# Performance work log

Hardware: AMD Instinct MI355X
Metric: run time of the kernel (lower is better)

## Reference

```python
import jax, jax.numpy as jnp
import numpy as np

C, H, W = 16, 512, 512
HID = 128
N_STEPS = 8


def setup_inputs() -> dict:
    key = jax.random.key(0)
    k1, k2, k3 = jax.random.split(key, 3)
    state = jax.random.normal(k1, (C, H, W), dtype=jnp.float32)
    # MLP params: 5*C = 80 gathered features -> HID -> C delta channels
    W1 = jax.random.normal(k2, (5 * C, HID), dtype=jnp.float32) * (1.0 / np.sqrt(5 * C))
    b1 = jnp.zeros((HID,), dtype=jnp.float32)
    W2 = jax.random.normal(k3, (HID, C), dtype=jnp.float32) * (1.0 / np.sqrt(HID))
    b2 = jnp.zeros((C,), dtype=jnp.float32)
    return {"state": state, "W1": W1, "b1": b1, "W2": W2, "b2": b2, "n_steps": N_STEPS}


def _neighbor_idx(n):
    i = jnp.arange(n)
    minus = jnp.maximum(i - 1, 0)          # clamp at low edge (cy==0 -> 0)
    plus = jnp.where(i == n - 1, 0, i + 1)  # WRAP to 0 at high edge (original quirk)
    return minus, plus


def reference(state, W1, b1, W2, b2, n_steps):
    c, h, w = state.shape
    up, down = _neighbor_idx(h)
    left, right = _neighbor_idx(w)

    def step(s, _):
        # von-Neumann gather: (5C, H, W), feature order [center, up, down, left, right]
        feats = jnp.concatenate(
            [s, s[:, up, :], s[:, down, :], s[:, :, left], s[:, :, right]], axis=0)
        x = feats.reshape(5 * c, h * w).T        # (HW, 5C)
        hdn = jax.nn.relu(x @ W1 + b1)           # (HW, HID)
        delta = (hdn @ W2 + b2).T.reshape(c, h, w)
        s_new = s + delta
        s_new = s_new.at[0].set(s[0])            # channel 0 snapshot restore
        return s_new, None

    out, _ = jax.lax.scan(step, state, None, length=n_steps)
    return out
```

## Files before the change

### kernel.cpp

```cpp
#include <hip/hip_runtime.h>
#include <hip/hip_bf16.h>

#define HH 512
#define WW 512
#define CC 16
#define HIDN 128
#define HWSZ (HH*WW)

typedef __attribute__((ext_vector_type(8))) short short8;
typedef __attribute__((ext_vector_type(4))) short short4v;
typedef __attribute__((ext_vector_type(4))) float float4v;

__device__ __forceinline__ short to_bf16(float f){
    __hip_bfloat16 h = __float2bfloat16(f);
    return __builtin_bit_cast(short, h);
}

__global__ void __launch_bounds__(256) prep_kernel(
    const float* __restrict__ W1, const float* __restrict__ W2,
    short* __restrict__ w1t, short* __restrict__ w2t)
{
    int t = blockIdx.x * blockDim.x + threadIdx.x;
    int stride = gridDim.x * blockDim.x;
    for (int idx = t; idx < HIDN*96; idx += stride){
        int n = idx / 96;
        int k = idx - n*96;
        float v = (k < 80) ? W1[k*HIDN + n] : 0.0f;
        w1t[idx] = to_bf16(v);
    }
    for (int idx = t; idx < CC*HIDN; idx += stride){
        int n = idx >> 7;
        int k = idx & 127;
        w2t[idx] = to_bf16(W2[k*CC + n]);
    }
}

#define RSTRIDE 24
#define RROW    (68*RSTRIDE)

__global__ void __launch_bounds__(256, 5) step_kernel(
    const float* __restrict__ src, float* __restrict__ dst,
    const short* __restrict__ w1t, const short* __restrict__ w2t,
    const float* __restrict__ b1, const float* __restrict__ b2)
{
    __shared__ __align__(16) short rows_u[3*RROW];
    __shared__ __align__(16) short hdn[64][136];

    const int t    = threadIdx.x;
    const int w    = t >> 6;
    const int lane = t & 63;
    const int ln15 = lane & 15;
    const int g4   = lane >> 4;

    const int bx = blockIdx.x;
    const int y  = bx >> 3;
    const int xs = (bx & 7) << 6;

    const int yu = (y == 0)      ? 0 : (y - 1);
    const int yd = (y == HH - 1) ? 0 : (y + 1);

    if (t < 192){
        const int r  = t >> 6;
        const int l  = t & 63;
        const int q  = l & 15;
        const int cq = l >> 4;
        const int rowg = (r == 0) ? y : ((r == 1) ? yu : yd);
        const float* base = src + (size_t)rowg * WW + xs + (q << 2);
        float4v f[4];
        #pragma unroll
        for (int i = 0; i < 4; ++i)
            f[i] = *(const float4v*)(base + (size_t)((cq << 2) + i) * HWSZ);
        #pragma unroll
        for (int j = 0; j < 4; ++j){
            short4v v;
            v[0] = to_bf16(f[0][j]); v[1] = to_bf16(f[1][j]);
            v[2] = to_bf16(f[2][j]); v[3] = to_bf16(f[3][j]);
            *(short4v*)&rows_u[r*RROW + ((q << 2) + 1 + j)*RSTRIDE + (cq << 2)] = v;
        }
    } else if (t < 224){
        const int c    = (t - 192) & 15;
        const int side = (t - 192) >> 4;
        const int gx   = (side == 0) ? ((xs == 0) ? 0 : xs - 1)
                                     : ((xs + 64 == WW) ? 0 : xs + 64);
        rows_u[(side * 65)*RSTRIDE + c] =
            to_bf16(src[(size_t)c*HWSZ + (size_t)y*WW + gx]);
    }

    int offB[3];
    #pragma unroll
    for (int kk = 0; kk < 3; ++kk){
        const int g  = (kk < 2) ? ((kk << 2) + g4) : (8 + (g4 & 1));
        const int n  = g >> 1;
        const int cb = (g & 1) << 3;
        const int r  = (n == 1) ? 1 : ((n == 2) ? 2 : 0);
        const int dx = (n == 3) ? -1 : ((n == 4) ? 1 : 0);
        offB[kk] = r*RROW + (ln15 + 1 + dx)*RSTRIDE + cb;
    }

    __syncthreads();

    float4v acc[2][4];
    #pragma unroll
    for (int mt = 0; mt < 2; ++mt)
        #pragma unroll
        for (int nt = 0; nt < 4; ++nt)
            acc[mt][nt] = (float4v){0.f, 0.f, 0.f, 0.f};

    #pragma unroll
    for (int kk = 0; kk < 3; ++kk){
        short8 bfragF[4];
        #pragma unroll
        for (int nt = 0; nt < 4; ++nt)
            bfragF[nt] = *(const short8*)(&rows_u[offB[kk] + nt * (16 * RSTRIDE)]);
        #pragma unroll
        for (int mt = 0; mt < 2; ++mt){
            const int hrow = (((w << 1) + mt) << 4) + ln15;
            short8 afragW = *(const short8*)(w1t + hrow * 96 + (kk << 5) + (g4 << 3));
            #pragma unroll
            for (int nt = 0; nt < 4; ++nt)
                acc[mt][nt] = __builtin_amdgcn_mfma_f32_16x16x32_bf16(
                    afragW, bfragF[nt], acc[mt][nt], 0, 0, 0);
        }
    }

    #pragma unroll
    for (int mt = 0; mt < 2; ++mt){
        const int hbase = (((w << 1) + mt) << 4) + (g4 << 2);
        const float4v bb = *(const float4v*)(b1 + hbase);
        #pragma unroll
        for (int nt = 0; nt < 4; ++nt){
            short4v s;
            #pragma unroll
            for (int r = 0; r < 4; ++r){
                float v = acc[mt][nt][r] + bb[r];
                v = v > 0.f ? v : 0.f;
                s[r] = to_bf16(v);
            }
            *(short4v*)&hdn[(nt << 4) + ln15][hbase] = s;
        }
    }
    __syncthreads();

    const int pxb = (w << 4) + (g4 << 2);
    const size_t gofs = (size_t)ln15 * HWSZ + (size_t)y * WW + xs + pxb;
    const float4v sold = *(const float4v*)(src + gofs);
    const float bias2 = b2[ln15];

    float4v acc2 = (float4v){0.f, 0.f, 0.f, 0.f};
    #pragma unroll
    for (int kk = 0; kk < 4; ++kk){
        const int k0 = kk << 5;
        short8 a = *(const short8*)(&hdn[(w << 4) + ln15][k0 + (g4 << 3)]);
        short8 b = *(const short8*)(w2t + ln15 * HIDN + k0 + (g4 << 3));
        acc2 = __builtin_amdgcn_mfma_f32_16x16x32_bf16(a, b, acc2, 0, 0, 0);
    }

    float4v outv;
    #pragma unroll
    for (int r = 0; r < 4; ++r){
        const float v = sold[r] + acc2[r] + bias2;
        outv[r] = (ln15 == 0) ? sold[r] : v;
    }
    *(float4v*)(dst + gofs) = outv;
}

extern "C" void kernel_launch(void* const* d_in, const int* in_sizes, int n_in,
                              void* d_out, int out_size, void* d_ws, size_t ws_size,
                              hipStream_t stream)
{
    const float* state = (const float*)d_in[0];
    const float* W1    = (const float*)d_in[1];
    const float* b1    = (const float*)d_in[2];
    const float* W2    = (const float*)d_in[3];
    const float* b2    = (const float*)d_in[4];

    float* B1  = (float*)d_ws;
    short* w1t = (short*)((char*)d_ws + (size_t)HWSZ * CC * 4);
    short* w2t = w1t + HIDN * 96;
    float* out = (float*)d_out;

    prep_kernel<<<32, 256, 0, stream>>>(W1, W2, w1t, w2t);

    dim3 grid(HH * (WW / 64));
    step_kernel<<<grid, 256, 0, stream>>>(state, B1, w1t, w2t, b1, b2);
    step_kernel<<<grid, 256, 0, stream>>>(B1, out, w1t, w2t, b1, b2);
    step_kernel<<<grid, 256, 0, stream>>>(out, B1, w1t, w2t, b1, b2);
    step_kernel<<<grid, 256, 0, stream>>>(B1, out, w1t, w2t, b1, b2);
    step_kernel<<<grid, 256, 0, stream>>>(out, B1, w1t, w2t, b1, b2);
    step_kernel<<<grid, 256, 0, stream>>>(B1, out, w1t, w2t, b1, b2);
    step_kernel<<<grid, 256, 0, stream>>>(out, B1, w1t, w2t, b1, b2);
    step_kernel<<<grid, 256, 0, stream>>>(B1, out, w1t, w2t, b1, b2);
}
```

Measured before the change: 264.2 us.

## Give each wave all hidden units for its own pixels, dropping a barrier

The first MLP layer is re-partitioned. Before, each wave computed 32 hidden units for all 64 pixels of the block. Now each wave computes all 128 hidden units for its own 16 pixels, so the hidden tile it writes to LDS is read back only by the same wave and the second __syncthreads can go. The staged-row LDS layout is compacted so up and down rows need no halo padding, and the launch-bounds occupancy hint rises from 5 to 6 blocks. In exchange, each wave now loads 8 W1 fragments per k-step instead of 2, raising cache traffic for weights, and it relies on in-wave LDS ordering with no explicit barrier.

```diff
diff --git a/kernel.cpp b/kernel.cpp
--- a/kernel.cpp
+++ b/kernel.cpp
@@ -36,14 +36,17 @@
 }
 
 #define RSTRIDE 24
-#define RROW    (68*RSTRIDE)
+#define BASE_C  0
+#define BASE_U  (66*RSTRIDE)
+#define BASE_D  ((66+64)*RSTRIDE)
+#define RTOT    ((66+64+64)*RSTRIDE)
 
-__global__ void __launch_bounds__(256, 5) step_kernel(
+__global__ void __launch_bounds__(256, 6) step_kernel(
     const float* __restrict__ src, float* __restrict__ dst,
     const short* __restrict__ w1t, const short* __restrict__ w2t,
     const float* __restrict__ b1, const float* __restrict__ b2)
 {
-    __shared__ __align__(16) short rows_u[3*RROW];
+    __shared__ __align__(16) short rows_u[RTOT];
     __shared__ __align__(16) short hdn[64][136];
 
     const int t    = threadIdx.x;
@@ -65,6 +68,8 @@
         const int q  = l & 15;
         const int cq = l >> 4;
         const int rowg = (r == 0) ? y : ((r == 1) ? yu : yd);
+        const int pbase = (r == 0) ? BASE_C : ((r == 1) ? BASE_U : BASE_D);
+        const int xoff  = (r == 0) ? 1 : 0;
         const float* base = src + (size_t)rowg * WW + xs + (q << 2);
         float4v f[4];
         #pragma unroll
@@ -75,14 +80,14 @@
             short4v v;
             v[0] = to_bf16(f[0][j]); v[1] = to_bf16(f[1][j]);
             v[2] = to_bf16(f[2][j]); v[3] = to_bf16(f[3][j]);
-            *(short4v*)&rows_u[r*RROW + ((q << 2) + 1 + j)*RSTRIDE + (cq << 2)] = v;
+            *(short4v*)&rows_u[pbase + ((q << 2) + xoff + j)*RSTRIDE + (cq << 2)] = v;
         }
     } else if (t < 224){
         const int c    = (t - 192) & 15;
         const int side = (t - 192) >> 4;
         const int gx   = (side == 0) ? ((xs == 0) ? 0 : xs - 1)
                                      : ((xs + 64 == WW) ? 0 : xs + 64);
-        rows_u[(side * 65)*RSTRIDE + c] =
+        rows_u[BASE_C + (side * 65)*RSTRIDE + c] =
             to_bf16(src[(size_t)c*HWSZ + (size_t)y*WW + gx]);
     }
 
@@ -92,66 +97,60 @@
         const int g  = (kk < 2) ? ((kk << 2) + g4) : (8 + (g4 & 1));
         const int n  = g >> 1;
         const int cb = (g & 1) << 3;
-        const int r  = (n == 1) ? 1 : ((n == 2) ? 2 : 0);
-        const int dx = (n == 3) ? -1 : ((n == 4) ? 1 : 0);
-        offB[kk] = r*RROW + (ln15 + 1 + dx)*RSTRIDE + cb;
+        int o;
+        if (n == 1)      o = BASE_U + ln15*RSTRIDE;
+        else if (n == 2) o = BASE_D + ln15*RSTRIDE;
+        else {
+            const int dx = (n == 3) ? -1 : ((n == 4) ? 1 : 0);
+            o = BASE_C + (ln15 + 1 + dx)*RSTRIDE;
+        }
+        offB[kk] = o + cb + w * (16 * RSTRIDE);
     }
+    const float bias2 = b2[ln15];
 
-    __syncthreads();
-
-    float4v acc[2][4];
-    #pragma unroll
-    for (int mt = 0; mt < 2; ++mt)
-        #pragma unroll
-        for (int nt = 0; nt < 4; ++nt)
-            acc[mt][nt] = (float4v){0.f, 0.f, 0.f, 0.f};
-
-    #pragma unroll
-    for (int kk = 0; kk < 3; ++kk){
-        short8 bfragF[4];
-        #pragma unroll
-        for (int nt = 0; nt < 4; ++nt)
-            bfragF[nt] = *(const short8*)(&rows_u[offB[kk] + nt * (16 * RSTRIDE)]);
-        #pragma unroll
-        for (int mt = 0; mt < 2; ++mt){
-            const int hrow = (((w << 1) + mt) << 4) + ln15;
-            short8 afragW = *(const short8*)(w1t + hrow * 96 + (kk << 5) + (g4 << 3));
-            #pragma unroll
-            for (int nt = 0; nt < 4; ++nt)
-                acc[mt][nt] = __builtin_amdgcn_mfma_f32_16x16x32_bf16(
-                    afragW, bfragF[nt], acc[mt][nt], 0, 0, 0);
-        }
-    }
-
-    #pragma unroll
-    for (int mt = 0; mt < 2; ++mt){
-        const int hbase = (((w << 1) + mt) << 4) + (g4 << 2);
-        const float4v bb = *(const float4v*)(b1 + hbase);
-        #pragma unroll
-        for (int nt = 0; nt < 4; ++nt){
-            short4v s;
-            #pragma unroll
-            for (int r = 0; r < 4; ++r){
-                float v = acc[mt][nt][r] + bb[r];
-                v = v > 0.f ? v : 0.f;
-                s[r] = to_bf16(v);
-            }
-            *(short4v*)&hdn[(nt << 4) + ln15][hbase] = s;
-        }
-    }
     __syncthreads();
 
     const int pxb = (w << 4) + (g4 << 2);
     const size_t gofs = (size_t)ln15 * HWSZ + (size_t)y * WW + xs + pxb;
     const float4v sold = *(const float4v*)(src + gofs);
-    const float bias2 = b2[ln15];
+
+    float4v acc[8];
+    #pragma unroll
+    for (int mt = 0; mt < 8; ++mt)
+        acc[mt] = (float4v){0.f, 0.f, 0.f, 0.f};
+
+    #pragma unroll
+    for (int kk = 0; kk < 3; ++kk){
+        const short8 bfragF = *(const short8*)(&rows_u[offB[kk]]);
+        #pragma unroll
+        for (int mt = 0; mt < 8; ++mt){
+            const int hrow = (mt << 4) + ln15;
+            const short8 afragW = *(const short8*)(w1t + hrow * 96 + (kk << 5) + (g4 << 3));
+            acc[mt] = __builtin_amdgcn_mfma_f32_16x16x32_bf16(
+                afragW, bfragF, acc[mt], 0, 0, 0);
+        }
+    }
+
+    #pragma unroll
+    for (int mt = 0; mt < 8; ++mt){
+        const int hbase = (mt << 4) + (g4 << 2);
+        const float4v bb = *(const float4v*)(b1 + hbase);
+        short4v s;
+        #pragma unroll
+        for (int r = 0; r < 4; ++r){
+            float v = acc[mt][r] + bb[r];
+            v = v > 0.f ? v : 0.f;
+            s[r] = to_bf16(v);
+        }
+        *(short4v*)&hdn[(w << 4) + ln15][hbase] = s;
+    }
 
     float4v acc2 = (float4v){0.f, 0.f, 0.f, 0.f};
     #pragma unroll
     for (int kk = 0; kk < 4; ++kk){
         const int k0 = kk << 5;
-        short8 a = *(const short8*)(&hdn[(w << 4) + ln15][k0 + (g4 << 3)]);
-        short8 b = *(const short8*)(w2t + ln15 * HIDN + k0 + (g4 << 3));
+        const short8 a = *(const short8*)(&hdn[(w << 4) + ln15][k0 + (g4 << 3)]);
+        const short8 b = *(const short8*)(w2t + ln15 * HIDN + k0 + (g4 << 3));
         acc2 = __builtin_amdgcn_mfma_f32_16x16x32_bf16(a, b, acc2, 0, 0, 0);
     }
 
@@ -170,9 +169,9 @@
 {
     const float* state = (const float*)d_in[0];
     const float* W1    = (const float*)d_in[1];
-    const float* b1    = (const float*)d_in[2];
+    const float* b1p   = (const float*)d_in[2];
     const float* W2    = (const float*)d_in[3];
-    const float* b2    = (const float*)d_in[4];
+    const float* b2p   = (const float*)d_in[4];
 
     float* B1  = (float*)d_ws;
     short* w1t = (short*)((char*)d_ws + (size_t)HWSZ * CC * 4);
@@ -182,12 +181,12 @@
     prep_kernel<<<32, 256, 0, stream>>>(W1, W2, w1t, w2t);
 
     dim3 grid(HH * (WW / 64));
-    step_kernel<<<grid, 256, 0, stream>>>(state, B1, w1t, w2t, b1, b2);
-    step_kernel<<<grid, 256, 0, stream>>>(B1, out, w1t, w2t, b1, b2);
-    step_kernel<<<grid, 256, 0, stream>>>(out, B1, w1t, w2t, b1, b2);
-    step_kernel<<<grid, 256, 0, stream>>>(B1, out, w1t, w2t, b1, b2);
-    step_kernel<<<grid, 256, 0, stream>>>(out, B1, w1t, w2t, b1, b2);
-    step_kernel<<<grid, 256, 0, stream>>>(B1, out, w1t, w2t, b1, b2);
-    step_kernel<<<grid, 256, 0, stream>>>(out, B1, w1t, w2t, b1, b2);
-    step_kernel<<<grid, 256, 0, stream>>>(B1, out, w1t, w2t, b1, b2);
+    step_kernel<<<grid, 256, 0, stream>>>(state, B1, w1t, w2t, b1p, b2p);
+    step_kernel<<<grid, 256, 0, stream>>>(B1, out, w1t, w2t, b1p, b2p);
+    step_kernel<<<grid, 256, 0, stream>>>(out, B1, w1t, w2t, b1p, b2p);
+    step_kernel<<<grid, 256, 0, stream>>>(B1, out, w1t, w2t, b1p, b2p);
+    step_kernel<<<grid, 256, 0, stream>>>(out, B1, w1t, w2t, b1p, b2p);
+    step_kernel<<<grid, 256, 0, stream>>>(B1, out, w1t, w2t, b1p, b2p);
+    step_kernel<<<grid, 256, 0, stream>>>(out, B1, w1t, w2t, b1p, b2p);
+    step_kernel<<<grid, 256, 0, stream>>>(B1, out, w1t, w2t, b1p, b2p);
 }
```

New measurement: 422.1 us. 1.6x slower.

## Write channel-interleaved bf16 state copy so next step gathers neighbors directly

Applied to the files above, without the earlier changes.

Each step now also writes a bf16 copy of its output in pixel-major, channel-interleaved layout (16 channels contiguous per pixel). Later steps load their MFMA B fragments straight from global memory through this copy, which removes the shared-memory staging of three rows, the fp32-to-bf16 conversion and the first barrier. The cost is an extra scattered 2-byte store per element each step, plus workspace for two bf16 buffers, with a fallback to the old path when the workspace is too small. The fp32 state is still read for the residual add.

```diff
diff --git a/kernel.cpp b/kernel.cpp
--- a/kernel.cpp
+++ b/kernel.cpp
@@ -38,8 +38,10 @@
 #define RSTRIDE 24
 #define RROW    (68*RSTRIDE)
 
-__global__ void __launch_bounds__(256, 5) step_kernel(
+template<bool WRITE_BF>
+__global__ void __launch_bounds__(256, 5) step_v2(
     const float* __restrict__ src, float* __restrict__ dst,
+    short* __restrict__ dstb,
     const short* __restrict__ w1t, const short* __restrict__ w2t,
     const float* __restrict__ b1, const float* __restrict__ b2)
 {
@@ -96,6 +98,7 @@
         const int dx = (n == 3) ? -1 : ((n == 4) ? 1 : 0);
         offB[kk] = r*RROW + (ln15 + 1 + dx)*RSTRIDE + cb;
     }
+    const float bias2 = b2[ln15];
 
     __syncthreads();
 
@@ -129,14 +132,14 @@
         const float4v bb = *(const float4v*)(b1 + hbase);
         #pragma unroll
         for (int nt = 0; nt < 4; ++nt){
-            short4v s;
+            short4v sv;
             #pragma unroll
             for (int r = 0; r < 4; ++r){
                 float v = acc[mt][nt][r] + bb[r];
                 v = v > 0.f ? v : 0.f;
-                s[r] = to_bf16(v);
+                sv[r] = to_bf16(v);
             }
-            *(short4v*)&hdn[(nt << 4) + ln15][hbase] = s;
+            *(short4v*)&hdn[(nt << 4) + ln15][hbase] = sv;
         }
     }
     __syncthreads();
@@ -144,15 +147,14 @@
     const int pxb = (w << 4) + (g4 << 2);
     const size_t gofs = (size_t)ln15 * HWSZ + (size_t)y * WW + xs + pxb;
     const float4v sold = *(const float4v*)(src + gofs);
-    const float bias2 = b2[ln15];
 
     float4v acc2 = (float4v){0.f, 0.f, 0.f, 0.f};
     #pragma unroll
     for (int kk = 0; kk < 4; ++kk){
         const int k0 = kk << 5;
         short8 a = *(const short8*)(&hdn[(w << 4) + ln15][k0 + (g4 << 3)]);
-        short8 b = *(const short8*)(w2t + ln15 * HIDN + k0 + (g4 << 3));
-        acc2 = __builtin_amdgcn_mfma_f32_16x16x32_bf16(a, b, acc2, 0, 0, 0);
+        short8 bb = *(const short8*)(w2t + ln15 * HIDN + k0 + (g4 << 3));
+        acc2 = __builtin_amdgcn_mfma_f32_16x16x32_bf16(a, bb, acc2, 0, 0, 0);
     }
 
     float4v outv;
@@ -162,6 +164,118 @@
         outv[r] = (ln15 == 0) ? sold[r] : v;
     }
     *(float4v*)(dst + gofs) = outv;
+
+    if constexpr (WRITE_BF){
+        #pragma unroll
+        for (int r = 0; r < 4; ++r)
+            dstb[((size_t)((y << 9) + xs + pxb + r) << 4) + ln15] = to_bf16(outv[r]);
+    }
+}
+
+template<bool WRITE_BF>
+__global__ void __launch_bounds__(256, 5) step_fast(
+    const float* __restrict__ srcf, const short* __restrict__ srcb,
+    float* __restrict__ dst, short* __restrict__ dstb,
+    const short* __restrict__ w1t, const short* __restrict__ w2t,
+    const float* __restrict__ b1, const float* __restrict__ b2)
+{
+    __shared__ __align__(16) short hdn[64][136];
+
+    const int t    = threadIdx.x;
+    const int w    = t >> 6;
+    const int lane = t & 63;
+    const int ln15 = lane & 15;
+    const int g4   = lane >> 4;
+
+    const int bx = blockIdx.x;
+    const int y  = bx >> 3;
+    const int xs = (bx & 7) << 6;
+
+    const int yu = (y == 0)      ? 0 : (y - 1);
+    const int yd = (y == HH - 1) ? 0 : (y + 1);
+
+    short8 bfragF[3][4];
+    #pragma unroll
+    for (int kk = 0; kk < 3; ++kk){
+        const int g  = (kk < 2) ? ((kk << 2) + g4) : (8 + (g4 & 1));
+        const int n  = g >> 1;
+        const int cb = (g & 1) << 3;
+        const int rowg = (n == 1) ? yu : ((n == 2) ? yd : y);
+        #pragma unroll
+        for (int nt = 0; nt < 4; ++nt){
+            const int c = xs + (nt << 4) + ln15;
+            const int colg = (n == 3) ? ((c == 0) ? 0 : c - 1)
+                          : ((n == 4) ? ((c == WW - 1) ? 0 : c + 1) : c);
+            bfragF[kk][nt] =
+                *(const short8*)(srcb + ((((size_t)rowg << 9) + colg) << 4) + cb);
+        }
+    }
+
+    const int pxb = (w << 4) + (g4 << 2);
+    const size_t gofs = (size_t)ln15 * HWSZ + (size_t)y * WW + xs + pxb;
+    const float4v sold = *(const float4v*)(srcf + gofs);
+    const float bias2 = b2[ln15];
+
+    float4v acc[2][4];
+    #pragma unroll
+    for (int mt = 0; mt < 2; ++mt)
+        #pragma unroll
+        for (int nt = 0; nt < 4; ++nt)
+            acc[mt][nt] = (float4v){0.f, 0.f, 0.f, 0.f};
+
+    #pragma unroll
+    for (int kk = 0; kk < 3; ++kk){
+        #pragma unroll
+        for (int mt = 0; mt < 2; ++mt){
+            const int hrow = (((w << 1) + mt) << 4) + ln15;
+            const short8 afragW = *(const short8*)(w1t + hrow * 96 + (kk << 5) + (g4 << 3));
+            #pragma unroll
+            for (int nt = 0; nt < 4; ++nt)
+                acc[mt][nt] = __builtin_amdgcn_mfma_f32_16x16x32_bf16(
+                    afragW, bfragF[kk][nt], acc[mt][nt], 0, 0, 0);
+        }
+    }
+
+    #pragma unroll
+    for (int mt = 0; mt < 2; ++mt){
+        const int hbase = (((w << 1) + mt) << 4) + (g4 << 2);
+        const float4v bb = *(const float4v*)(b1 + hbase);
+        #pragma unroll
+        for (int nt = 0; nt < 4; ++nt){
+            short4v sv;
+            #pragma unroll
+            for (int r = 0; r < 4; ++r){
+                float v = acc[mt][nt][r] + bb[r];
+                v = v > 0.f ? v : 0.f;
+                sv[r] = to_bf16(v);
+            }
+            *(short4v*)&hdn[(nt << 4) + ln15][hbase] = sv;
+        }
+    }
+    __syncthreads();
+
+    float4v acc2 = (float4v){0.f, 0.f, 0.f, 0.f};
+    #pragma unroll
+    for (int kk = 0; kk < 4; ++kk){
+        const int k0 = kk << 5;
+        const short8 a  = *(const short8*)(&hdn[(w << 4) + ln15][k0 + (g4 << 3)]);
+        const short8 bb = *(const short8*)(w2t + ln15 * HIDN + k0 + (g4 << 3));
+        acc2 = __builtin_amdgcn_mfma_f32_16x16x32_bf16(a, bb, acc2, 0, 0, 0);
+    }
+
+    float4v outv;
+    #pragma unroll
+    for (int r = 0; r < 4; ++r){
+        const float v = sold[r] + acc2[r] + bias2;
+        outv[r] = (ln15 == 0) ? sold[r] : v;
+    }
+    *(float4v*)(dst + gofs) = outv;
+
+    if constexpr (WRITE_BF){
+        #pragma unroll
+        for (int r = 0; r < 4; ++r)
+            dstb[((size_t)((y << 9) + xs + pxb + r) << 4) + ln15] = to_bf16(outv[r]);
+    }
 }
 
 extern "C" void kernel_launch(void* const* d_in, const int* in_sizes, int n_in,
@@ -170,24 +284,42 @@
 {
     const float* state = (const float*)d_in[0];
     const float* W1    = (const float*)d_in[1];
-    const float* b1    = (const float*)d_in[2];
+    const float* b1p   = (const float*)d_in[2];
     const float* W2    = (const float*)d_in[3];
-    const float* b2    = (const float*)d_in[4];
+    const float* b2p   = (const float*)d_in[4];
 
     float* B1  = (float*)d_ws;
     short* w1t = (short*)((char*)d_ws + (size_t)HWSZ * CC * 4);
     short* w2t = w1t + HIDN * 96;
+    short* bfA = w2t + CC * HIDN;
+    short* bfB = bfA + (size_t)HWSZ * CC;
     float* out = (float*)d_out;
 
+    const size_t need = (size_t)HWSZ*CC*4
+                      + (size_t)(HIDN*96 + CC*HIDN)*2
+                      + (size_t)HWSZ*CC*2*2;
+
     prep_kernel<<<32, 256, 0, stream>>>(W1, W2, w1t, w2t);
 
     dim3 grid(HH * (WW / 64));
-    step_kernel<<<grid, 256, 0, stream>>>(state, B1, w1t, w2t, b1, b2);
-    step_kernel<<<grid, 256, 0, stream>>>(B1, out, w1t, w2t, b1, b2);
-    step_kernel<<<grid, 256, 0, stream>>>(out, B1, w1t, w2t, b1, b2);
-    step_kernel<<<grid, 256, 0, stream>>>(B1, out, w1t, w2t, b1, b2);
-    step_kernel<<<grid, 256, 0, stream>>>(out, B1, w1t, w2t, b1, b2);
-    step_kernel<<<grid, 256, 0, stream>>>(B1, out, w1t, w2t, b1, b2);
-    step_kernel<<<grid, 256, 0, stream>>>(out, B1, w1t, w2t, b1, b2);
-    step_kernel<<<grid, 256, 0, stream>>>(B1, out, w1t, w2t, b1, b2);
-}
+
+    if (ws_size >= need){
+        step_v2<true>  <<<grid, 256, 0, stream>>>(state, B1, bfA, w1t, w2t, b1p, b2p);
+        step_fast<true> <<<grid, 256, 0, stream>>>(B1,  bfA, out, bfB, w1t, w2t, b1p, b2p);
+        step_fast<true> <<<grid, 256, 0, stream>>>(out, bfB, B1,  bfA, w1t, w2t, b1p, b2p);
+        step_fast<true> <<<grid, 256, 0, stream>>>(B1,  bfA, out, bfB, w1t, w2t, b1p, b2p);
+        step_fast<true> <<<grid, 256, 0, stream>>>(out, bfB, B1,  bfA, w1t, w2t, b1p, b2p);
+        step_fast<true> <<<grid, 256, 0, stream>>>(B1,  bfA, out, bfB, w1t, w2t, b1p, b2p);
+        step_fast<true> <<<grid, 256, 0, stream>>>(out, bfB, B1,  bfA, w1t, w2t, b1p, b2p);
+        step_fast<false><<<grid, 256, 0, stream>>>(B1,  bfA, out, nullptr, w1t, w2t, b1p, b2p);
+    } else {
+        step_v2<false><<<grid, 256, 0, stream>>>(state, B1, nullptr, w1t, w2t, b1p, b2p);
+        step_v2<false><<<grid, 256, 0, stream>>>(B1, out, nullptr, w1t, w2t, b1p, b2p);
+        step_v2<false><<<grid, 256, 0, stream>>>(out, B1, nullptr, w1t, w2t, b1p, b2p);
+        step_v2<false><<<grid, 256, 0, stream>>>(B1, out, nullptr, w1t, w2t, b1p, b2p);
+        step_v2<false><<<grid, 256, 0, stream>>>(out, B1, nullptr, w1t, w2t, b1p, b2p);
+        step_v2<false><<<grid, 256, 0, stream>>>(B1, out, nullptr, w1t, w2t, b1p, b2p);
+        step_v2<false><<<grid, 256, 0, stream>>>(out, B1, nullptr, w1t, w2t, b1p, b2p);
+        step_v2<false><<<grid, 256, 0, stream>>>(B1, out, nullptr, w1t, w2t, b1p, b2p);
+    }
+}
```

After: 283.7 us. 1.07x slower.
